# Performance work log

Measured on AMD Instinct MI355X. Metric: run time of the kernel, lower is better.

## Reference

```python
import jax, jax.numpy as jnp
import numpy as np

N_NODES = 100000
N_EDGES = 1600000
F_IN = 512
HIDDEN = 16
N_CLASSES = 40


def gcn_conv(x, edge_index, W, b, n_nodes):
    # PyG GCNConv: h = x @ W, add self-loops, sym-normalize, scatter-add, + bias
    h = x @ W  # [N, F_out]
    row, col = edge_index[0], edge_index[1]
    # add self-loops
    loop = jnp.arange(n_nodes, dtype=row.dtype)
    row = jnp.concatenate([row, loop])
    col = jnp.concatenate([col, loop])
    # degree of destination nodes (with self-loops)
    deg = jax.ops.segment_sum(jnp.ones_like(col, dtype=h.dtype), col,
                              num_segments=n_nodes)
    deg_inv_sqrt = jnp.where(deg > 0, jax.lax.rsqrt(deg), 0.0)
    norm = deg_inv_sqrt[row] * deg_inv_sqrt[col]  # [E+N]
    msg = h[row] * norm[:, None]  # gather + scale
    out = jax.ops.segment_sum(msg, col, num_segments=n_nodes)  # scatter-add
    return out + b


def setup_inputs() -> dict:
    key = jax.random.key(0)
    k1, k2, k3, k4 = jax.random.split(key, 4)
    x = jax.random.normal(k1, (N_NODES, F_IN), dtype=jnp.float32)
    edge_index = jax.random.randint(k2, (2, N_EDGES), 0, N_NODES, dtype=jnp.int64)
    # Glorot-style init for weights, zeros for biases (as PyG GCNConv)
    W1 = jax.random.normal(k3, (F_IN, HIDDEN), dtype=jnp.float32) / np.sqrt(F_IN)
    b1 = jnp.zeros((HIDDEN,), dtype=jnp.float32)
    W2 = jax.random.normal(k4, (HIDDEN, N_CLASSES), dtype=jnp.float32) / np.sqrt(HIDDEN)
    b2 = jnp.zeros((N_CLASSES,), dtype=jnp.float32)
    return {"x": x, "edge_index": edge_index, "W1": W1, "b1": b1,
            "W2": W2, "b2": b2}


def reference(x, edge_index, W1, b1, W2, b2):
    n = x.shape[0]
    h = gcn_conv(x, edge_index, W1, b1, n)
    h = jax.nn.relu(h)
    out = gcn_conv(h, edge_index, W2, b2, n)
    return out
```

## Files before the change

### kernel.cpp

```cpp
#include <hip/hip_runtime.h>

#define N_NODES 100000
#define N_EDGES 1600000
#define F_IN    512
#define HIDDEN  16
#define N_CLS   40

#define BSHIFT  7
#define BSIZE   128
#define NB      ((N_NODES + BSIZE - 1) / BSIZE)
#define NWGBIN  256
#define CHUNK   (N_EDGES / NWGBIN)

static_assert(N_EDGES % NWGBIN == 0, "chunking must be exact");

__global__ void k_zero(int* __restrict__ p, int n) {
    int i = blockIdx.x * blockDim.x + threadIdx.x;
    if (i < n) p[i] = 0;
}

__global__ __launch_bounds__(256) void k_binc(const int* __restrict__ ei,
                                              int* __restrict__ bucketCnt) {
    __shared__ int h[NB];
    int t = threadIdx.x;
    for (int b = t; b < NB; b += 256) h[b] = 0;
    __syncthreads();
    int start = blockIdx.x * CHUNK, end = start + CHUNK;
    for (int e = start + t; e < end; e += 256)
        atomicAdd(&h[ei[N_EDGES + e] >> BSHIFT], 1);
    __syncthreads();
    for (int b = t; b < NB; b += 256)
        if (h[b]) atomicAdd(&bucketCnt[b], h[b]);
}

__global__ __launch_bounds__(1024) void k_bscan(const int* __restrict__ bucketCnt,
                                                int* __restrict__ boff,
                                                int* __restrict__ cur) {
    __shared__ int s[1024];
    int t = threadIdx.x;
    int v = (t < NB) ? bucketCnt[t] : 0;
    s[t] = v; __syncthreads();
    for (int o = 1; o < 1024; o <<= 1) {
        int add = (t >= o) ? s[t - o] : 0;
        __syncthreads();
        s[t] += add;
        __syncthreads();
    }
    if (t < NB) { int ex = s[t] - v; boff[t] = ex; cur[t] = ex; }
    if (t == 0) boff[NB] = N_EDGES;
}

__global__ __launch_bounds__(256) void k_bfill(const int* __restrict__ ei,
                                               int* __restrict__ cur,
                                               int* __restrict__ binned) {
    __shared__ int lc[NB];
    int t = threadIdx.x;
    int start = blockIdx.x * CHUNK, end = start + CHUNK;
    for (int b = t; b < NB; b += 256) lc[b] = 0;
    __syncthreads();
    for (int e = start + t; e < end; e += 256)
        atomicAdd(&lc[ei[N_EDGES + e] >> BSHIFT], 1);
    __syncthreads();
    for (int b = t; b < NB; b += 256) {
        int c = lc[b];
        lc[b] = c ? atomicAdd(&cur[b], c) : 0;
    }
    __syncthreads();
    for (int e = start + t; e < end; e += 256) {
        int r = ei[e], c = ei[N_EDGES + e];
        int b = c >> BSHIFT;
        int pos = atomicAdd(&lc[b], 1);
        binned[pos] = r | ((c & (BSIZE - 1)) << 17);
    }
}

__global__ __launch_bounds__(256) void k_csr(const int* __restrict__ boff,
                                             const int* __restrict__ binned,
                                             int* __restrict__ csr,
                                             int* __restrict__ offsets,
                                             int* __restrict__ cnt,
                                             float* __restrict__ dis) {
    __shared__ int h[BSIZE];
    __shared__ int sc[BSIZE];
    __shared__ int curL[BSIZE];
    int t = threadIdx.x, b = blockIdx.x;
    if (t < BSIZE) h[t] = 0;
    __syncthreads();
    int s = boff[b], e = boff[b + 1];
    for (int i = s + t; i < e; i += 256)
        atomicAdd(&h[binned[i] >> 17], 1);
    __syncthreads();
    int v = (t < BSIZE) ? h[t] : 0;
    if (t < BSIZE) sc[t] = v;
    __syncthreads();
    for (int o = 1; o < BSIZE; o <<= 1) {
        int add = (t < BSIZE && t >= o) ? sc[t - o] : 0;
        __syncthreads();
        if (t < BSIZE) sc[t] += add;
        __syncthreads();
    }
    if (t < BSIZE) {
        int ex = s + sc[t] - v;
        curL[t] = ex;
        int node = b * BSIZE + t;
        if (node < N_NODES) {
            offsets[node] = ex;
            cnt[node]     = v;
            dis[node]     = rsqrtf(1.0f + (float)v);
        }
    }
    __syncthreads();
    for (int i = s + t; i < e; i += 256) {
        int p = binned[i];
        int pos = atomicAdd(&curL[p >> 17], 1);
        csr[pos] = p & 0x1FFFF;
    }
}

__global__ __launch_bounds__(256) void k_gemm1(
        const float* __restrict__ x, const float* __restrict__ W1,
        const float* __restrict__ dis, float* __restrict__ h1s) {
    __shared__ float sW[F_IN * 20];
    for (int idx = threadIdx.x; idx < F_IN * HIDDEN; idx += 256) {
        int k = idx >> 4, j = idx & 15;
        sW[k * 20 + j] = W1[idx];
    }
    __syncthreads();

    int t = threadIdx.x;
    int q = t & 3;
    int row0 = blockIdx.x * 128 + (t >> 2);
    int row1 = row0 + 64;
    bool ok0 = row0 < N_NODES, ok1 = row1 < N_NODES;
    const float* x0 = x + (size_t)row0 * F_IN;
    const float* x1 = x + (size_t)row1 * F_IN;

    float acc[2][16];
#pragma unroll
    for (int rr = 0; rr < 2; ++rr)
#pragma unroll
        for (int j = 0; j < 16; ++j) acc[rr][j] = 0.0f;

#pragma unroll 2
    for (int i = 0; i < 32; ++i) {
        int k0 = i * 16 + q * 4;
        float4 xv0 = ok0 ? *(const float4*)(x0 + k0) : float4{0, 0, 0, 0};
        float4 xv1 = ok1 ? *(const float4*)(x1 + k0) : float4{0, 0, 0, 0};
#pragma unroll
        for (int kk = 0; kk < 4; ++kk) {
            const float* wr = &sW[(k0 + kk) * 20];
            float4 w0 = *(const float4*)(wr);
            float4 w1 = *(const float4*)(wr + 4);
            float4 w2 = *(const float4*)(wr + 8);
            float4 w3 = *(const float4*)(wr + 12);
            float xs0 = (&xv0.x)[kk], xs1 = (&xv1.x)[kk];
            acc[0][0]  = fmaf(xs0, w0.x, acc[0][0]);   acc[1][0]  = fmaf(xs1, w0.x, acc[1][0]);
            acc[0][1]  = fmaf(xs0, w0.y, acc[0][1]);   acc[1][1]  = fmaf(xs1, w0.y, acc[1][1]);
            acc[0][2]  = fmaf(xs0, w0.z, acc[0][2]);   acc[1][2]  = fmaf(xs1, w0.z, acc[1][2]);
            acc[0][3]  = fmaf(xs0, w0.w, acc[0][3]);   acc[1][3]  = fmaf(xs1, w0.w, acc[1][3]);
            acc[0][4]  = fmaf(xs0, w1.x, acc[0][4]);   acc[1][4]  = fmaf(xs1, w1.x, acc[1][4]);
            acc[0][5]  = fmaf(xs0, w1.y, acc[0][5]);   acc[1][5]  = fmaf(xs1, w1.y, acc[1][5]);
            acc[0][6]  = fmaf(xs0, w1.z, acc[0][6]);   acc[1][6]  = fmaf(xs1, w1.z, acc[1][6]);
            acc[0][7]  = fmaf(xs0, w1.w, acc[0][7]);   acc[1][7]  = fmaf(xs1, w1.w, acc[1][7]);
            acc[0][8]  = fmaf(xs0, w2.x, acc[0][8]);   acc[1][8]  = fmaf(xs1, w2.x, acc[1][8]);
            acc[0][9]  = fmaf(xs0, w2.y, acc[0][9]);   acc[1][9]  = fmaf(xs1, w2.y, acc[1][9]);
            acc[0][10] = fmaf(xs0, w2.z, acc[0][10]);  acc[1][10] = fmaf(xs1, w2.z, acc[1][10]);
            acc[0][11] = fmaf(xs0, w2.w, acc[0][11]);  acc[1][11] = fmaf(xs1, w2.w, acc[1][11]);
            acc[0][12] = fmaf(xs0, w3.x, acc[0][12]);  acc[1][12] = fmaf(xs1, w3.x, acc[1][12]);
            acc[0][13] = fmaf(xs0, w3.y, acc[0][13]);  acc[1][13] = fmaf(xs1, w3.y, acc[1][13]);
            acc[0][14] = fmaf(xs0, w3.z, acc[0][14]);  acc[1][14] = fmaf(xs1, w3.z, acc[1][14]);
            acc[0][15] = fmaf(xs0, w3.w, acc[0][15]);  acc[1][15] = fmaf(xs1, w3.w, acc[1][15]);
        }
    }

#pragma unroll
    for (int rr = 0; rr < 2; ++rr) {
        float t16[16];
#pragma unroll
        for (int j = 0; j < 16; ++j)
            t16[j] = acc[rr][j] + __shfl_xor(acc[rr][j], 2);
        float k8[8];
#pragma unroll
        for (int j = 0; j < 8; ++j)
            k8[j] = (q & 2) ? t16[8 + j] : t16[j];
        float t8[8];
#pragma unroll
        for (int j = 0; j < 8; ++j)
            t8[j] = k8[j] + __shfl_xor(k8[j], 1);
#pragma unroll
        for (int j = 0; j < 4; ++j)
            acc[rr][j] = (q & 1) ? t8[4 + j] : t8[j];
    }

    if (ok0) {
        float d = dis[row0];
        *(float4*)(h1s + (size_t)row0 * HIDDEN + q * 4) =
            { acc[0][0] * d, acc[0][1] * d, acc[0][2] * d, acc[0][3] * d };
    }
    if (ok1) {
        float d = dis[row1];
        *(float4*)(h1s + (size_t)row1 * HIDDEN + q * 4) =
            { acc[1][0] * d, acc[1][1] * d, acc[1][2] * d, acc[1][3] * d };
    }
}

__global__ __launch_bounds__(256) void k_agg1(
        const int* __restrict__ offsets, const int* __restrict__ cnt,
        const int* __restrict__ csr, const float* __restrict__ dis,
        const float* __restrict__ b1,
        const float* __restrict__ h1s, float* __restrict__ g) {
    int t = blockIdx.x * 256 + threadIdx.x;
    int node = t >> 2;
    if (node >= N_NODES) return;
    int q = t & 3;
    int lanebase = (threadIdx.x & 63) & ~3;

    float4 acc = *(const float4*)(h1s + (size_t)node * HIDDEN + q * 4);
    int start = offsets[node];
    int n = cnt[node];
    int i = 0;
    for (; i + 4 <= n; i += 4) {
        int rv = csr[start + i + q];
#pragma unroll
        for (int j = 0; j < 4; ++j) {
            int r = __shfl(rv, lanebase + j);
            float4 v = *(const float4*)(h1s + (size_t)r * HIDDEN + q * 4);
            acc.x += v.x; acc.y += v.y; acc.z += v.z; acc.w += v.w;
        }
    }
    for (; i < n; ++i) {
        int r = csr[start + i];
        float4 v = *(const float4*)(h1s + (size_t)r * HIDDEN + q * 4);
        acc.x += v.x; acc.y += v.y; acc.z += v.z; acc.w += v.w;
    }
    float d = dis[node];
    float4 bq = *(const float4*)(b1 + q * 4);
    float4 r;
    r.x = fmaxf(fmaf(acc.x, d, bq.x), 0.0f) * d;
    r.y = fmaxf(fmaf(acc.y, d, bq.y), 0.0f) * d;
    r.z = fmaxf(fmaf(acc.z, d, bq.z), 0.0f) * d;
    r.w = fmaxf(fmaf(acc.w, d, bq.w), 0.0f) * d;
    *(float4*)(g + (size_t)node * HIDDEN + q * 4) = r;
}

__global__ __launch_bounds__(256) void k_agg2(
        const int* __restrict__ offsets, const int* __restrict__ cnt,
        const int* __restrict__ csr, const float* __restrict__ dis,
        const float* __restrict__ W2, const float* __restrict__ b2,
        const float* __restrict__ g, float* __restrict__ out) {
    __shared__ float sW[HIDDEN * N_CLS];
    __shared__ float sb2[N_CLS];
    __shared__ float sAgg[64][HIDDEN + 1];
    int t = threadIdx.x;
    for (int i = t; i < HIDDEN * N_CLS; i += 256) sW[i] = W2[i];
    if (t < N_CLS) sb2[t] = b2[t];

    int gt = blockIdx.x * 256 + t;
    int node = gt >> 2;
    int q = t & 3;
    int ln = t >> 2;
    int lanebase = (t & 63) & ~3;

    if (node < N_NODES) {
        float4 acc = *(const float4*)(g + (size_t)node * HIDDEN + q * 4);
        int start = offsets[node];
        int n = cnt[node];
        int i = 0;
        for (; i + 4 <= n; i += 4) {
            int rv = csr[start + i + q];
#pragma unroll
            for (int j = 0; j < 4; ++j) {
                int r = __shfl(rv, lanebase + j);
                float4 v = *(const float4*)(g + (size_t)r * HIDDEN + q * 4);
                acc.x += v.x; acc.y += v.y; acc.z += v.z; acc.w += v.w;
            }
        }
        for (; i < n; ++i) {
            int r = csr[start + i];
            float4 v = *(const float4*)(g + (size_t)r * HIDDEN + q * 4);
            acc.x += v.x; acc.y += v.y; acc.z += v.z; acc.w += v.w;
        }
        float d = dis[node];
        sAgg[ln][q*4+0] = acc.x * d;
        sAgg[ln][q*4+1] = acc.y * d;
        sAgg[ln][q*4+2] = acc.z * d;
        sAgg[ln][q*4+3] = acc.w * d;
    }
    __syncthreads();
    if (node >= N_NODES) return;

    float a[HIDDEN];
#pragma unroll
    for (int j = 0; j < HIDDEN; ++j) a[j] = sAgg[ln][j];

    int c0 = q * 10;
    float o[10];
#pragma unroll
    for (int k = 0; k < 10; ++k) o[k] = sb2[c0 + k];
#pragma unroll
    for (int j = 0; j < HIDDEN; ++j) {
        float aj = a[j];
        const float* wr = &sW[j * N_CLS + c0];
#pragma unroll
        for (int k = 0; k < 10; ++k) o[k] = fmaf(aj, wr[k], o[k]);
    }
    float* op = out + (size_t)node * N_CLS + c0;
#pragma unroll
    for (int k = 0; k < 10; ++k) op[k] = o[k];
}

extern "C" void kernel_launch(void* const* d_in, const int* in_sizes, int n_in,
                              void* d_out, int out_size, void* d_ws, size_t ws_size,
                              hipStream_t stream) {
    const float* x  = (const float*)d_in[0];
    const int*   ei = (const int*)d_in[1];
    const float* W1 = (const float*)d_in[2];
    const float* b1 = (const float*)d_in[3];
    const float* W2 = (const float*)d_in[4];
    const float* b2 = (const float*)d_in[5];
    float* out = (float*)d_out;

    char* w = (char*)d_ws;
    int*   bucketCnt = (int*)w;    w += 784 * 4;
    int*   boff      = (int*)w;    w += 784 * 4;
    int*   cur       = (int*)w;    w += 784 * 4;
    int*   offsets   = (int*)w;    w += (size_t)N_NODES * 4;
    int*   cnt       = (int*)w;    w += (size_t)N_NODES * 4;
    float* dis       = (float*)w;  w += (size_t)N_NODES * 4;
    int*   binned    = (int*)w;    w += (size_t)N_EDGES * 4;
    int*   csr       = (int*)w;    w += (size_t)N_EDGES * 4;
    float* h1s       = (float*)w;  w += (size_t)N_NODES * HIDDEN * 4;
    float* g         = (float*)w;

    const int gGemm = (N_NODES + 127) / 128;
    const int gAgg  = (N_NODES * 4 + 255) / 256;

    k_zero <<<(NB + 255) / 256, 256, 0, stream>>>(bucketCnt, NB);
    k_binc <<<NWGBIN, 256, 0, stream>>>(ei, bucketCnt);
    k_bscan<<<1, 1024, 0, stream>>>(bucketCnt, boff, cur);
    k_bfill<<<NWGBIN, 256, 0, stream>>>(ei, cur, binned);
    k_csr  <<<NB, 256, 0, stream>>>(boff, binned, csr, offsets, cnt, dis);
    k_gemm1<<<gGemm, 256, 0, stream>>>(x, W1, dis, h1s);
    k_agg1 <<<gAgg, 256, 0, stream>>>(offsets, cnt, csr, dis, b1, h1s, g);
    k_agg2 <<<gAgg, 256, 0, stream>>>(offsets, cnt, csr, dis, W2, b2, g, out);
}
```

Before: 453.8 us.

## Compute first-layer GEMM with split-bf16 MFMA instead of FP32 FMAs

The x@W1 projection now runs on matrix cores. Each FP32 value is split into a high and a low bf16 part, and three 16x16x32 bf16 MFMAs per k-step (hi*hi, hi*lo, lo*hi) approximate FP32 accuracy. W1 is staged in LDS as swizzled hi/lo bf16 arrays, and x loads are software-prefetched two k-tiles ahead. The aim is to remove the scalar-FMA compute bound so the kernel is limited by reading x, at the cost of per-element conversion ALU work and a small loss of precision.

```diff
diff --git a/kernel.cpp b/kernel.cpp
--- a/kernel.cpp
+++ b/kernel.cpp
@@ -13,6 +13,9 @@
 #define CHUNK   (N_EDGES / NWGBIN)
 
 static_assert(N_EDGES % NWGBIN == 0, "chunking must be exact");
+
+typedef __attribute__((ext_vector_type(8))) short bf16x8;
+typedef __attribute__((ext_vector_type(4))) float f32x4;
 
 __global__ void k_zero(int* __restrict__ p, int n) {
     int i = blockIdx.x * blockDim.x + threadIdx.x;
@@ -120,87 +123,76 @@
 __global__ __launch_bounds__(256) void k_gemm1(
         const float* __restrict__ x, const float* __restrict__ W1,
         const float* __restrict__ dis, float* __restrict__ h1s) {
-    __shared__ float sW[F_IN * 20];
-    for (int idx = threadIdx.x; idx < F_IN * HIDDEN; idx += 256) {
-        int k = idx >> 4, j = idx & 15;
-        sW[k * 20 + j] = W1[idx];
-    }
-    __syncthreads();
-
-    int t = threadIdx.x;
-    int q = t & 3;
-    int row0 = blockIdx.x * 128 + (t >> 2);
-    int row1 = row0 + 64;
-    bool ok0 = row0 < N_NODES, ok1 = row1 < N_NODES;
-    const float* x0 = x + (size_t)row0 * F_IN;
-    const float* x1 = x + (size_t)row1 * F_IN;
-
-    float acc[2][16];
-#pragma unroll
-    for (int rr = 0; rr < 2; ++rr)
-#pragma unroll
-        for (int j = 0; j < 16; ++j) acc[rr][j] = 0.0f;
-
-#pragma unroll 2
-    for (int i = 0; i < 32; ++i) {
-        int k0 = i * 16 + q * 4;
-        float4 xv0 = ok0 ? *(const float4*)(x0 + k0) : float4{0, 0, 0, 0};
-        float4 xv1 = ok1 ? *(const float4*)(x1 + k0) : float4{0, 0, 0, 0};
-#pragma unroll
-        for (int kk = 0; kk < 4; ++kk) {
-            const float* wr = &sW[(k0 + kk) * 20];
-            float4 w0 = *(const float4*)(wr);
-            float4 w1 = *(const float4*)(wr + 4);
-            float4 w2 = *(const float4*)(wr + 8);
-            float4 w3 = *(const float4*)(wr + 12);
-            float xs0 = (&xv0.x)[kk], xs1 = (&xv1.x)[kk];
-            acc[0][0]  = fmaf(xs0, w0.x, acc[0][0]);   acc[1][0]  = fmaf(xs1, w0.x, acc[1][0]);
-            acc[0][1]  = fmaf(xs0, w0.y, acc[0][1]);   acc[1][1]  = fmaf(xs1, w0.y, acc[1][1]);
-            acc[0][2]  = fmaf(xs0, w0.z, acc[0][2]);   acc[1][2]  = fmaf(xs1, w0.z, acc[1][2]);
-            acc[0][3]  = fmaf(xs0, w0.w, acc[0][3]);   acc[1][3]  = fmaf(xs1, w0.w, acc[1][3]);
-            acc[0][4]  = fmaf(xs0, w1.x, acc[0][4]);   acc[1][4]  = fmaf(xs1, w1.x, acc[1][4]);
-            acc[0][5]  = fmaf(xs0, w1.y, acc[0][5]);   acc[1][5]  = fmaf(xs1, w1.y, acc[1][5]);
-            acc[0][6]  = fmaf(xs0, w1.z, acc[0][6]);   acc[1][6]  = fmaf(xs1, w1.z, acc[1][6]);
-            acc[0][7]  = fmaf(xs0, w1.w, acc[0][7]);   acc[1][7]  = fmaf(xs1, w1.w, acc[1][7]);
-            acc[0][8]  = fmaf(xs0, w2.x, acc[0][8]);   acc[1][8]  = fmaf(xs1, w2.x, acc[1][8]);
-            acc[0][9]  = fmaf(xs0, w2.y, acc[0][9]);   acc[1][9]  = fmaf(xs1, w2.y, acc[1][9]);
-            acc[0][10] = fmaf(xs0, w2.z, acc[0][10]);  acc[1][10] = fmaf(xs1, w2.z, acc[1][10]);
-            acc[0][11] = fmaf(xs0, w2.w, acc[0][11]);  acc[1][11] = fmaf(xs1, w2.w, acc[1][11]);
-            acc[0][12] = fmaf(xs0, w3.x, acc[0][12]);  acc[1][12] = fmaf(xs1, w3.x, acc[1][12]);
-            acc[0][13] = fmaf(xs0, w3.y, acc[0][13]);  acc[1][13] = fmaf(xs1, w3.y, acc[1][13]);
-            acc[0][14] = fmaf(xs0, w3.z, acc[0][14]);  acc[1][14] = fmaf(xs1, w3.z, acc[1][14]);
-            acc[0][15] = fmaf(xs0, w3.w, acc[0][15]);  acc[1][15] = fmaf(xs1, w3.w, acc[1][15]);
-        }
-    }
-
-#pragma unroll
-    for (int rr = 0; rr < 2; ++rr) {
-        float t16[16];
-#pragma unroll
-        for (int j = 0; j < 16; ++j)
-            t16[j] = acc[rr][j] + __shfl_xor(acc[rr][j], 2);
-        float k8[8];
-#pragma unroll
-        for (int j = 0; j < 8; ++j)
-            k8[j] = (q & 2) ? t16[8 + j] : t16[j];
-        float t8[8];
-#pragma unroll
-        for (int j = 0; j < 8; ++j)
-            t8[j] = k8[j] + __shfl_xor(k8[j], 1);
-#pragma unroll
-        for (int j = 0; j < 4; ++j)
-            acc[rr][j] = (q & 1) ? t8[4 + j] : t8[j];
-    }
-
-    if (ok0) {
-        float d = dis[row0];
-        *(float4*)(h1s + (size_t)row0 * HIDDEN + q * 4) =
-            { acc[0][0] * d, acc[0][1] * d, acc[0][2] * d, acc[0][3] * d };
-    }
-    if (ok1) {
-        float d = dis[row1];
-        *(float4*)(h1s + (size_t)row1 * HIDDEN + q * 4) =
-            { acc[1][0] * d, acc[1][1] * d, acc[1][2] * d, acc[1][3] * d };
+    __shared__ short sWhi[F_IN * HIDDEN];
+    __shared__ short sWlo[F_IN * HIDDEN];
+    int t = threadIdx.x;
+    for (int idx = t; idx < F_IN * HIDDEN; idx += 256) {
+        int k = idx >> 4, n = idx & 15;
+        float f = W1[idx];
+        unsigned u  = __float_as_uint(f);
+        unsigned rh = u + 0x7FFFu + ((u >> 16) & 1u);
+        float fh = __uint_as_float(rh & 0xFFFF0000u);
+        float fl = f - fh;
+        unsigned v  = __float_as_uint(fl);
+        unsigned rl = v + 0x7FFFu + ((v >> 16) & 1u);
+        int p = (n * F_IN + k) ^ ((n & 7) << 3);
+        sWhi[p] = (short)(rh >> 16);
+        sWlo[p] = (short)(rl >> 16);
+    }
+    __syncthreads();
+
+    int bid = blockIdx.x * 4 + (t >> 6);
+    if (bid >= N_NODES / 16) return;
+    int l  = t & 63;
+    int n  = l & 15;
+    int ko = (l >> 4) << 3;
+    const float* xp = x + (size_t)(bid * 16 + n) * F_IN + ko;
+    const int xsw = (n & 7) << 3;
+    const int nb  = n * F_IN;
+
+    f32x4 accA = {0.f, 0.f, 0.f, 0.f};
+    f32x4 accB = {0.f, 0.f, 0.f, 0.f};
+
+    float4 pA0 = *(const float4*)(xp + 0);
+    float4 pB0 = *(const float4*)(xp + 4);
+    float4 pA1 = *(const float4*)(xp + 32);
+    float4 pB1 = *(const float4*)(xp + 36);
+
+#pragma unroll
+    for (int kt = 0; kt < 16; ++kt) {
+        float4 a = (kt & 1) ? pA1 : pA0;
+        float4 b = (kt & 1) ? pB1 : pB0;
+        if (kt + 2 < 16) {
+            const float4* src0 = (const float4*)(xp + (kt + 2) * 32);
+            const float4* src1 = (const float4*)(xp + (kt + 2) * 32 + 4);
+            if (kt & 1) { pA1 = *src0; pB1 = *src1; }
+            else        { pA0 = *src0; pB0 = *src1; }
+        }
+        float fs[8] = {a.x, a.y, a.z, a.w, b.x, b.y, b.z, b.w};
+        bf16x8 ah, al;
+#pragma unroll
+        for (int e = 0; e < 8; ++e) {
+            unsigned u  = __float_as_uint(fs[e]);
+            unsigned rh = u + 0x7FFFu + ((u >> 16) & 1u);
+            ah[e] = (short)(rh >> 16);
+            float fl = fs[e] - __uint_as_float(rh & 0xFFFF0000u);
+            unsigned v  = __float_as_uint(fl);
+            unsigned rl = v + 0x7FFFu + ((v >> 16) & 1u);
+            al[e] = (short)(rl >> 16);
+        }
+        int p = (nb + kt * 32 + ko) ^ xsw;
+        bf16x8 bh = *(const bf16x8*)(sWhi + p);
+        bf16x8 bl = *(const bf16x8*)(sWlo + p);
+        accA = __builtin_amdgcn_mfma_f32_16x16x32_bf16(ah, bh, accA, 0, 0, 0);
+        accB = __builtin_amdgcn_mfma_f32_16x16x32_bf16(ah, bl, accB, 0, 0, 0);
+        accB = __builtin_amdgcn_mfma_f32_16x16x32_bf16(al, bh, accB, 0, 0, 0);
+    }
+
+    int mrow = bid * 16 + ((l >> 4) << 2);
+#pragma unroll
+    for (int r = 0; r < 4; ++r) {
+        float d = dis[mrow + r];
+        h1s[(size_t)(mrow + r) * HIDDEN + n] = (accA[r] + accB[r]) * d;
     }
 }
 
@@ -332,7 +324,7 @@
     float* h1s       = (float*)w;  w += (size_t)N_NODES * HIDDEN * 4;
     float* g         = (float*)w;
 
-    const int gGemm = (N_NODES + 127) / 128;
+    const int gGemm = (N_NODES / 16 + 3) / 4;
     const int gAgg  = (N_NODES * 4 + 255) / 256;
 
     k_zero <<<(NB + 255) / 256, 256, 0, stream>>>(bucketCnt, NB);
```

New measurement: 421.3 us. 7.2% less time.
